# Optimization experiments

Hardware: AMD Instinct MI355X
Metric: run time of the kernel (lower is better)

The kernel has to match this reference:

```python
import jax, jax.numpy as jnp
import numpy as np

N = 50000
E = 800000
IN_CH = 128
HID = 16
HEADS = 8
OUT_CH = 64
NEG_SLOPE = 0.2


def _gat_conv(x, src, dst, W, a_src, a_dst, b, heads, ch):
    # x: [N, F_in]; W: [F_in, heads*ch]; a_src/a_dst: [heads, ch]; b: [heads*ch] or [ch]
    n = x.shape[0]
    h = (x @ W).reshape(n, heads, ch)                      # [N, H, C]
    s = jnp.einsum('nhc,hc->nh', h, a_src)                 # [N, H]
    d = jnp.einsum('nhc,hc->nh', h, a_dst)                 # [N, H]
    e = jax.nn.leaky_relu(s[src] + d[dst], NEG_SLOPE)      # [E, H]
    # numerically stable segment softmax over destination neighborhoods
    m = jax.ops.segment_max(e, dst, num_segments=n)        # [N, H]
    m = jnp.where(jnp.isfinite(m), m, 0.0)                 # guard isolated nodes
    w = jnp.exp(e - m[dst])                                # [E, H]
    z = jax.ops.segment_sum(w, dst, num_segments=n)        # [N, H]
    alpha = w / (z[dst] + 1e-16)                           # [E, H]
    msg = h[src] * alpha[:, :, None]                       # [E, H, C]
    out = jax.ops.segment_sum(msg, dst, num_segments=n)    # [N, H, C]
    return out.reshape(n, heads * ch) + b


def setup_inputs() -> dict:
    key = jax.random.key(0)
    ks = jax.random.split(key, 10)
    x = jax.random.normal(ks[0], (N, IN_CH), dtype=jnp.float32)
    edge_index = jax.random.randint(ks[1], (2, E), 0, N, dtype=jnp.int64)
    g1 = 1.0 / np.sqrt(IN_CH)
    g2 = 1.0 / np.sqrt(HEADS * HID)
    W1 = jax.random.normal(ks[2], (IN_CH, HEADS * HID), dtype=jnp.float32) * g1
    a_src1 = jax.random.normal(ks[3], (HEADS, HID), dtype=jnp.float32) * g2
    a_dst1 = jax.random.normal(ks[4], (HEADS, HID), dtype=jnp.float32) * g2
    b1 = jnp.zeros((HEADS * HID,), dtype=jnp.float32)
    W2 = jax.random.normal(ks[5], (HEADS * HID, OUT_CH), dtype=jnp.float32) * g2
    a_src2 = jax.random.normal(ks[6], (1, OUT_CH), dtype=jnp.float32) * (1.0 / np.sqrt(OUT_CH))
    a_dst2 = jax.random.normal(ks[7], (1, OUT_CH), dtype=jnp.float32) * (1.0 / np.sqrt(OUT_CH))
    b2 = jnp.zeros((OUT_CH,), dtype=jnp.float32)
    return {"x": x, "edge_index": edge_index,
            "W1": W1, "a_src1": a_src1, "a_dst1": a_dst1, "b1": b1,
            "W2": W2, "a_src2": a_src2, "a_dst2": a_dst2, "b2": b2}


def reference(x, edge_index, W1, a_src1, a_dst1, b1, W2, a_src2, a_dst2, b2):
    src, dst = edge_index[0], edge_index[1]
    # dropout layers are identity at inference
    h = _gat_conv(x, src, dst, W1, a_src1, a_dst1, b1, HEADS, HID)
    h = jax.nn.elu(h)
    out = _gat_conv(h, src, dst, W2, a_src2, a_dst2, b2, 1, OUT_CH)
    return out
```

## Files before the change

### kernel.cpp

```cpp
#include <hip/hip_runtime.h>
#include <hip/hip_fp16.h>

#define INCH   128
#define HEADS1 8
#define HID1   16
#define C1     128
#define C2     64
#define NEG_SLOPE 0.2f
#define SB     256

using f16x8 = __attribute__((ext_vector_type(8))) _Float16;
using f32x4 = __attribute__((ext_vector_type(4))) float;

__device__ __forceinline__ float lrelu(float v) { return v >= 0.f ? v : NEG_SLOPE * v; }
__device__ __forceinline__ int swzA(int row, int byteInRow) {
  return (row << 8) | (byteInRow ^ ((row & 15) << 4));
}


__global__ void prep_kernel(const float* __restrict__ x, __half* __restrict__ xh,
                            const float* __restrict__ W1, __half* __restrict__ W1t,
                            const float* __restrict__ W2, __half* __restrict__ W2t,
                            const int* __restrict__ dst, int* __restrict__ deg,
                            int cvtB, int tB, int total8, int E) {
  const int b = blockIdx.x, t = threadIdx.x;
  if (b < cvtB) {
    int i = b * 256 + t;
    if (i >= total8) return;
    const float4* p = (const float4*)x + (size_t)i * 2;
    float4 v0 = p[0], v1 = p[1];
    __half2 ha = __floats2half2_rn(v0.x, v0.y);
    __half2 hb = __floats2half2_rn(v0.z, v0.w);
    __half2 hc = __floats2half2_rn(v1.x, v1.y);
    __half2 hd = __floats2half2_rn(v1.z, v1.w);
    uint4 w = { *(unsigned*)&ha, *(unsigned*)&hb, *(unsigned*)&hc, *(unsigned*)&hd };
    ((uint4*)xh)[i] = w;
  } else if (b < cvtB + tB) {
    int id = (b - cvtB) * 256 + t;
    if (id < 128 * 128) {
      int col = id >> 7, k = id & 127;
      W1t[id] = __float2half(W1[k * 128 + col]);
    } else if (id < 128 * 128 + 64 * 128) {
      int idx = id - 128 * 128;
      int col = idx >> 7, k = idx & 127;
      W2t[idx] = __float2half(W2[k * 64 + col]);
    }
  } else {
    int e = (b - cvtB - tB) * 256 + t;
    if (e < E) atomicAdd(&deg[dst[e]], 1);
  }
}


__global__ void scan1_kernel(const int* __restrict__ deg, int* __restrict__ partial, int N) {
  __shared__ int sh[SB];
  const int b = blockIdx.x, t = threadIdx.x;
  const int chunk = (N + SB - 1) / SB;
  const int lo = b * chunk, hi = min(lo + chunk, N);
  int s = 0;
  for (int i = lo + t; i < hi; i += SB) s += deg[i];
  sh[t] = s;
  __syncthreads();
  for (int off = SB / 2; off; off >>= 1) {
    if (t < off) sh[t] += sh[t + off];
    __syncthreads();
  }
  if (t == 0) partial[b] = sh[0];
}

__global__ void scan3_kernel(const int* __restrict__ deg, const int* __restrict__ partial,
                             int* __restrict__ row_start, int N) {
  __shared__ int pref[SB];
  __shared__ int sh[SB];
  const int b = blockIdx.x, t = threadIdx.x;
  int pv = partial[t];
  pref[t] = pv;
  __syncthreads();
  for (int off = 1; off < SB; off <<= 1) {
    int u = (t >= off) ? pref[t - off] : 0;
    __syncthreads();
    pref[t] += u;
    __syncthreads();
  }
  const int chunk = (N + SB - 1) / SB;
  const int lo = b * chunk, hi = min(lo + chunk, N);
  int run = (b == 0) ? 0 : pref[b - 1];
  for (int base = lo; base < hi; base += SB) {
    int i = base + t;
    int v = (i < hi) ? deg[i] : 0;
    sh[t] = v;
    __syncthreads();
    for (int off = 1; off < SB; off <<= 1) {
      int u = (t >= off) ? sh[t - off] : 0;
      __syncthreads();
      sh[t] += u;
      __syncthreads();
    }
    if (i < hi) row_start[i] = run + sh[t] - v;
    run += sh[SB - 1];
    __syncthreads();
  }
  if (b == SB - 1 && t == 0) row_start[N] = run;
}

__global__ void fill_kernel(const int* __restrict__ src, const int* __restrict__ dst,
                            const int* __restrict__ row_start, int* __restrict__ cursor,
                            int* __restrict__ src_sorted, int E) {
  int e = blockIdx.x * blockDim.x + threadIdx.x;
  if (e >= E) return;
  int d = dst[e];
  int slot = row_start[d] + atomicAdd(&cursor[d], 1);
  src_sorted[slot] = src[e];
}

__global__ __launch_bounds__(256) void gemm1_mfma(
    const __half* __restrict__ xh, const __half* __restrict__ W1t,
    const float* __restrict__ a_src, const float* __restrict__ a_dst,
    __half* __restrict__ h1, float* __restrict__ s1, float* __restrict__ d1, int M) {
  __shared__ unsigned char As[16384];
  __shared__ unsigned char Bs[32768];
  const int t = threadIdx.x;
  const int m0 = blockIdx.x * 64;
  for (int c = t; c < 1024; c += 256) {
    int row = c >> 4, seg = c & 15;
    int gr = m0 + row;
    uint4 v = make_uint4(0, 0, 0, 0);
    if (gr < M) v = ((const uint4*)xh)[(unsigned)(gr << 4) + seg];
    *(uint4*)(As + swzA(row, seg << 4)) = v;
  }
  for (int c = t; c < 2048; c += 256) {
    int row = c >> 4, seg = c & 15;
    uint4 v = ((const uint4*)W1t)[(row << 4) + seg];
    *(uint4*)(Bs + swzA(row, seg << 4)) = v;
  }
  __syncthreads();
  const int l = t & 63, wid = t >> 6;
  const int c16 = l & 15;
  const int kOff = (l >> 4) << 4;
  const int rA = (wid << 4) | c16;
  f16x8 a[4];
#pragma unroll
  for (int kb = 0; kb < 4; ++kb)
    a[kb] = *(const f16x8*)(As + swzA(rA, (kb << 6) + kOff));
#pragma unroll
  for (int ct = 0; ct < 8; ++ct) {
    const int rB = (ct << 4) | c16;
    f32x4 acc = {0.f, 0.f, 0.f, 0.f};
#pragma unroll
    for (int kb = 0; kb < 4; ++kb) {
      f16x8 b = *(const f16x8*)(Bs + swzA(rB, (kb << 6) + kOff));
      acc = __builtin_amdgcn_mfma_f32_16x16x32_f16(a[kb], b, acc, 0, 0, 0);
    }
    const int colg = (ct << 4) + c16;
    const float asv = a_src[colg], adv = a_dst[colg];
#pragma unroll
    for (int i = 0; i < 4; ++i) {
      const int n = m0 + (wid << 4) + ((l >> 4) << 2) + i;
      float v = acc[i];
      float sv = v * asv, dv = v * adv;
      sv += __shfl_xor(sv, 1); sv += __shfl_xor(sv, 2);
      sv += __shfl_xor(sv, 4); sv += __shfl_xor(sv, 8);
      dv += __shfl_xor(dv, 1); dv += __shfl_xor(dv, 2);
      dv += __shfl_xor(dv, 4); dv += __shfl_xor(dv, 8);
      if (n < M) {
        h1[(unsigned)(n << 7) + colg] = __float2half(v);
        if (c16 == 0) { s1[n * HEADS1 + ct] = sv; d1[n * HEADS1 + ct] = dv; }
      }
    }
  }
}

__global__ __launch_bounds__(256) void gemm2_mfma(
    const __half* __restrict__ x2h, const __half* __restrict__ W2t,
    const float* __restrict__ a_src, const float* __restrict__ a_dst,
    __half* __restrict__ h2, float* __restrict__ s2, float* __restrict__ d2, int M) {
  __shared__ unsigned char As[16384];
  __shared__ unsigned char Bs[16384];
  const int t = threadIdx.x;
  const int m0 = blockIdx.x * 64;
  for (int c = t; c < 1024; c += 256) {
    int row = c >> 4, seg = c & 15;
    int gr = m0 + row;
    uint4 v = make_uint4(0, 0, 0, 0);
    if (gr < M) v = ((const uint4*)x2h)[(unsigned)(gr << 4) + seg];
    *(uint4*)(As + swzA(row, seg << 4)) = v;
  }
  for (int c = t; c < 1024; c += 256) {
    int row = c >> 4, seg = c & 15;
    uint4 v = ((const uint4*)W2t)[(row << 4) + seg];
    *(uint4*)(Bs + swzA(row, seg << 4)) = v;
  }
  __syncthreads();
  const int l = t & 63, wid = t >> 6;
  const int c16 = l & 15;
  const int kOff = (l >> 4) << 4;
  const int rA = (wid << 4) | c16;
  f16x8 a[4];
#pragma unroll
  for (int kb = 0; kb < 4; ++kb)
    a[kb] = *(const f16x8*)(As + swzA(rA, (kb << 6) + kOff));
  float svp[4] = {0.f, 0.f, 0.f, 0.f};
  float dvp[4] = {0.f, 0.f, 0.f, 0.f};
#pragma unroll
  for (int ct = 0; ct < 4; ++ct) {
    const int rB = (ct << 4) | c16;
    f32x4 acc = {0.f, 0.f, 0.f, 0.f};
#pragma unroll
    for (int kb = 0; kb < 4; ++kb) {
      f16x8 b = *(const f16x8*)(Bs + swzA(rB, (kb << 6) + kOff));
      acc = __builtin_amdgcn_mfma_f32_16x16x32_f16(a[kb], b, acc, 0, 0, 0);
    }
    const int colg = (ct << 4) + c16;
    const float asv = a_src[colg], adv = a_dst[colg];
#pragma unroll
    for (int i = 0; i < 4; ++i) {
      const int n = m0 + (wid << 4) + ((l >> 4) << 2) + i;
      float v = acc[i];
      svp[i] += v * asv;
      dvp[i] += v * adv;
      if (n < M) h2[(unsigned)(n << 6) + colg] = __float2half(v);
    }
  }
#pragma unroll
  for (int i = 0; i < 4; ++i) {
    float sv = svp[i], dv = dvp[i];
    sv += __shfl_xor(sv, 1); sv += __shfl_xor(sv, 2);
    sv += __shfl_xor(sv, 4); sv += __shfl_xor(sv, 8);
    dv += __shfl_xor(dv, 1); dv += __shfl_xor(dv, 2);
    dv += __shfl_xor(dv, 4); dv += __shfl_xor(dv, 8);
    const int n = m0 + (wid << 4) + ((l >> 4) << 2) + i;
    if (c16 == 0 && n < M) { s2[n] = sv; d2[n] = dv; }
  }
}

__global__ __launch_bounds__(256) void layer1_agg(
    const int* __restrict__ row_start, const int* __restrict__ src_sorted,
    const float* __restrict__ s1, const float* __restrict__ d1,
    const __half* __restrict__ h1, const float* __restrict__ b1,
    __half* __restrict__ x2h, int N) {
  __shared__ float wlds[4][64][8];
  const int wv = threadIdx.x >> 6;
  const int lane = threadIdx.x & 63;
  const int le = lane >> 3, h = lane & 7;
  const int es = lane >> 4, cl = lane & 15;
  const int hh = cl >> 1;
  const uint4* __restrict__ h1v = (const uint4*)h1;
  const int waveId = blockIdx.x * 4 + wv;
  const int stride = gridDim.x * 4;
  for (int n = waveId; n < N; n += stride) {
    const int lo = row_start[n], hi = row_start[n + 1];
    const float dv = d1[n * HEADS1 + h];
    float z = 0.f;
    float acc[8] = {0.f, 0.f, 0.f, 0.f, 0.f, 0.f, 0.f, 0.f};
    for (int base = lo; base < hi; base += 64) {
      const int cnt = min(64, hi - base);
      const int c1 = cnt - 1;
      const int j0 = le, j1 = 8 + le;
      const int sj0 = src_sorted[base + min(j0, c1)];
      const int sj1 = src_sorted[base + min(j1, c1)];
      const float sv0 = s1[sj0 * HEADS1 + h];
      const float sv1 = s1[sj1 * HEADS1 + h];
      const int ps0 = src_sorted[base + min(es, c1)];
      const int ps1 = src_sorted[base + min(4 + es, c1)];
      const int ps2 = src_sorted[base + min(8 + es, c1)];
      const int ps3 = src_sorted[base + min(12 + es, c1)];
      const uint4 pf0 = h1v[(unsigned)(ps0 << 4) + cl];
      const uint4 pf1 = h1v[(unsigned)(ps1 << 4) + cl];
      const uint4 pf2 = h1v[(unsigned)(ps2 << 4) + cl];
      const uint4 pf3 = h1v[(unsigned)(ps3 << 4) + cl];
      const float w0 = (j0 < cnt) ? __expf(lrelu(sv0 + dv)) : 0.f;
      const float w1 = (j1 < cnt) ? __expf(lrelu(sv1 + dv)) : 0.f;
      z += w0 + w1;
      const int rmax = (cnt + 7) >> 3;
      for (int r = 2; r < rmax; ++r) {
        const int j = (r << 3) + le;
        float w = 0.f;
        if (j < cnt) w = __expf(lrelu(s1[src_sorted[base + j] * HEADS1 + h] + dv));
        wlds[wv][j][h] = w;
        z += w;
      }
      {
        const float wA = __shfl(w0, (es << 3) | hh);
        const float wB = __shfl(w0, ((4 + es) << 3) | hh);
        const __half2* pA = (const __half2*)&pf0;
        const __half2* pB = (const __half2*)&pf1;
#pragma unroll
        for (int k = 0; k < 4; ++k) {
          float2 a2 = __half22float2(pA[k]);
          float2 b2v = __half22float2(pB[k]);
          acc[2 * k]     += wA * a2.x + wB * b2v.x;
          acc[2 * k + 1] += wA * a2.y + wB * b2v.y;
        }
      }
      if (cnt > 8) {
        const float wA = __shfl(w1, (es << 3) | hh);
        const float wB = __shfl(w1, ((4 + es) << 3) | hh);
        const __half2* pA = (const __half2*)&pf2;
        const __half2* pB = (const __half2*)&pf3;
#pragma unroll
        for (int k = 0; k < 4; ++k) {
          float2 a2 = __half22float2(pA[k]);
          float2 b2v = __half22float2(pB[k]);
          acc[2 * k]     += wA * a2.x + wB * b2v.x;
          acc[2 * k + 1] += wA * a2.y + wB * b2v.y;
        }
      }
      for (int i = 16; i < cnt; i += 8) {
        const int jA = i + es, jB = i + 4 + es;
        const float wA = wlds[wv][jA][hh];
        const float wB = wlds[wv][jB][hh];
        const int sA = src_sorted[base + min(jA, c1)];
        const int sB = src_sorted[base + min(jB, c1)];
        const uint4 fA = h1v[(unsigned)(sA << 4) + cl];
        const uint4 fB = h1v[(unsigned)(sB << 4) + cl];
        const __half2* pA = (const __half2*)&fA;
        const __half2* pB = (const __half2*)&fB;
#pragma unroll
        for (int k = 0; k < 4; ++k) {
          float2 a2 = __half22float2(pA[k]);
          float2 b2v = __half22float2(pB[k]);
          acc[2 * k]     += wA * a2.x + wB * b2v.x;
          acc[2 * k + 1] += wA * a2.y + wB * b2v.y;
        }
      }
    }
    z += __shfl_xor(z, 8); z += __shfl_xor(z, 16); z += __shfl_xor(z, 32);
    const float zsel = __shfl(z, hh);
#pragma unroll
    for (int k = 0; k < 8; ++k) {
      acc[k] += __shfl_xor(acc[k], 16);
      acc[k] += __shfl_xor(acc[k], 32);
    }
    if (es == 0) {
      const float zinv = 1.f / (zsel + 1e-16f);
      __half2 o[4];
#pragma unroll
      for (int k = 0; k < 4; ++k) {
        float ox = acc[2 * k] * zinv + b1[(cl << 3) + 2 * k];
        float oy = acc[2 * k + 1] * zinv + b1[(cl << 3) + 2 * k + 1];
        ox = ox > 0.f ? ox : expm1f(ox);
        oy = oy > 0.f ? oy : expm1f(oy);
        o[k] = __floats2half2_rn(ox, oy);
      }
      ((uint4*)x2h)[(unsigned)(n << 4) + cl] = *(const uint4*)o;
    }
  }
}

__global__ __launch_bounds__(256) void layer2_agg(
    const int* __restrict__ row_start, const int* __restrict__ src_sorted,
    const float* __restrict__ s2, const float* __restrict__ d2,
    const __half* __restrict__ h2, const float* __restrict__ b2,
    float* __restrict__ out, int N) {
  const int wv = threadIdx.x >> 6;
  const int lane = threadIdx.x & 63;
  const int es = lane >> 3, cl = lane & 7;
  const uint4* __restrict__ h2v = (const uint4*)h2;
  const int waveId = blockIdx.x * 4 + wv;
  const int stride = gridDim.x * 4;
  for (int n = waveId; n < N; n += stride) {
    const int lo = row_start[n], hi = row_start[n + 1];
    const float dv = d2[n];
    float z = 0.f;
    float acc[8] = {0.f, 0.f, 0.f, 0.f, 0.f, 0.f, 0.f, 0.f};
    for (int base = lo; base < hi; base += 64) {
      const int cnt = min(64, hi - base);
      const int c1 = cnt - 1;
      const int sidx = src_sorted[base + min(lane, c1)];
      const float sval = s2[sidx];
      const int ps0 = src_sorted[base + min(es, c1)];
      const int ps1 = src_sorted[base + min(8 + es, c1)];
      const int ps2 = src_sorted[base + min(16 + es, c1)];
      const int ps3 = src_sorted[base + min(24 + es, c1)];
      const uint4 pf0 = h2v[(unsigned)(ps0 << 3) + cl];
      const uint4 pf1 = h2v[(unsigned)(ps1 << 3) + cl];
      const uint4 pf2 = h2v[(unsigned)(ps2 << 3) + cl];
      const uint4 pf3 = h2v[(unsigned)(ps3 << 3) + cl];
      const float w = (lane < cnt) ? __expf(lrelu(sval + dv)) : 0.f;
      z += w;
      {
        const float wA = __shfl(w, es);
        const float wB = __shfl(w, 8 + es);
        const __half2* pA = (const __half2*)&pf0;
        const __half2* pB = (const __half2*)&pf1;
#pragma unroll
        for (int k = 0; k < 4; ++k) {
          float2 a2 = __half22float2(pA[k]);
          float2 b2v = __half22float2(pB[k]);
          acc[2 * k]     += wA * a2.x + wB * b2v.x;
          acc[2 * k + 1] += wA * a2.y + wB * b2v.y;
        }
      }
      if (cnt > 16) {
        const float wA = __shfl(w, 16 + es);
        const float wB = __shfl(w, 24 + es);
        const __half2* pA = (const __half2*)&pf2;
        const __half2* pB = (const __half2*)&pf3;
#pragma unroll
        for (int k = 0; k < 4; ++k) {
          float2 a2 = __half22float2(pA[k]);
          float2 b2v = __half22float2(pB[k]);
          acc[2 * k]     += wA * a2.x + wB * b2v.x;
          acc[2 * k + 1] += wA * a2.y + wB * b2v.y;
        }
      }
      for (int i = 32; i < cnt; i += 16) {
        const int jA = i + es, jB = i + 8 + es;
        const float wA = __shfl(w, jA);
        const float wB = __shfl(w, jB);
        const int sA = src_sorted[base + min(jA, c1)];
        const int sB = src_sorted[base + min(jB, c1)];
        const uint4 fA = h2v[(unsigned)(sA << 3) + cl];
        const uint4 fB = h2v[(unsigned)(sB << 3) + cl];
        const __half2* pA = (const __half2*)&fA;
        const __half2* pB = (const __half2*)&fB;
#pragma unroll
        for (int k = 0; k < 4; ++k) {
          float2 a2 = __half22float2(pA[k]);
          float2 b2v = __half22float2(pB[k]);
          acc[2 * k]     += wA * a2.x + wB * b2v.x;
          acc[2 * k + 1] += wA * a2.y + wB * b2v.y;
        }
      }
    }
#pragma unroll
    for (int off = 1; off < 64; off <<= 1) z += __shfl_xor(z, off);
#pragma unroll
    for (int k = 0; k < 8; ++k) {
      acc[k] += __shfl_xor(acc[k], 8);
      acc[k] += __shfl_xor(acc[k], 16);
      acc[k] += __shfl_xor(acc[k], 32);
    }
    if (es == 0) {
      const float zinv = 1.f / (z + 1e-16f);
      float4 o0, o1;
      o0.x = acc[0] * zinv + b2[(cl << 3) + 0];
      o0.y = acc[1] * zinv + b2[(cl << 3) + 1];
      o0.z = acc[2] * zinv + b2[(cl << 3) + 2];
      o0.w = acc[3] * zinv + b2[(cl << 3) + 3];
      o1.x = acc[4] * zinv + b2[(cl << 3) + 4];
      o1.y = acc[5] * zinv + b2[(cl << 3) + 5];
      o1.z = acc[6] * zinv + b2[(cl << 3) + 6];
      o1.w = acc[7] * zinv + b2[(cl << 3) + 7];
      float4* po = (float4*)&out[(unsigned)(n << 6) + (cl << 3)];
      po[0] = o0;
      po[1] = o1;
    }
  }
}

extern "C" void kernel_launch(void* const* d_in, const int* in_sizes, int n_in,
                              void* d_out, int out_size, void* d_ws, size_t ws_size,
                              hipStream_t stream) {
  const float* x      = (const float*)d_in[0];
  const int*   ei     = (const int*)d_in[1];
  const float* W1     = (const float*)d_in[2];
  const float* a_src1 = (const float*)d_in[3];
  const float* a_dst1 = (const float*)d_in[4];
  const float* b1     = (const float*)d_in[5];
  const float* W2     = (const float*)d_in[6];
  const float* a_src2 = (const float*)d_in[7];
  const float* a_dst2 = (const float*)d_in[8];
  const float* b2     = (const float*)d_in[9];
  float* out = (float*)d_out;

  const int N = in_sizes[0] / INCH;
  const int E = in_sizes[1] / 2;
  const int* src = ei;
  const int* dst = ei + E;

  float* ws = (float*)d_ws;
  size_t o = 0;
  __half* xh  = (__half*)(ws + o); o += (size_t)N * C1 / 2;
  __half* h1  = (__half*)(ws + o); o += (size_t)N * C1 / 2;
  __half* x2h = (__half*)(ws + o); o += (size_t)N * C1 / 2;
  float*  s1  = ws + o;            o += (size_t)N * HEADS1;
  float*  d1  = ws + o;            o += (size_t)N * HEADS1;
  __half* W1t = (__half*)(ws + o); o += 128 * 128 / 2;
  __half* W2t = (__half*)(ws + o); o += 64 * 128 / 2;
  int* deg        = (int*)(ws + o); o += N;
  int* cursor     = (int*)(ws + o); o += N;
  int* row_start  = (int*)(ws + o); o += N + 1;
  int* partial    = (int*)(ws + o); o += SB;
  int* src_sorted = (int*)(ws + o); o += E;
  __half* h2 = h1;
  float*  s2 = (float*)h1 + (size_t)N * 32;
  float*  d2 = s2 + N;

  const int EB = (E + 255) / 256;
  const int NB64 = (N + 63) / 64;
  const int total8 = N * C1 / 8;
  const int cvtB = (total8 + 255) / 256;
  const int tB = (128 * 128 + 64 * 128 + 255) / 256;
  const int histB = EB;
  const int AGGB = min((N + 3) / 4, 2048);

  hipMemsetAsync(deg, 0, (size_t)N * 4, stream);
  hipMemsetAsync(cursor, 0, (size_t)N * 4, stream);

  prep_kernel<<<cvtB + tB + histB, 256, 0, stream>>>(x, xh, W1, W1t, W2, W2t, dst, deg,
                                                     cvtB, tB, total8, E);
  scan1_kernel<<<SB, SB, 0, stream>>>(deg, partial, N);
  scan3_kernel<<<SB, SB, 0, stream>>>(deg, partial, row_start, N);
  fill_kernel<<<EB, 256, 0, stream>>>(src, dst, row_start, cursor, src_sorted, E);

  gemm1_mfma<<<NB64, 256, 0, stream>>>(xh, W1t, a_src1, a_dst1, h1, s1, d1, N);
  layer1_agg<<<AGGB, 256, 0, stream>>>(row_start, src_sorted, s1, d1, h1, b1, x2h, N);

  gemm2_mfma<<<NB64, 256, 0, stream>>>(x2h, W2t, a_src2, a_dst2, h2, s2, d2, N);
  layer2_agg<<<AGGB, 256, 0, stream>>>(row_start, src_sorted, s2, d2, h2, b2, out, N);
}
```

Before: 197.3 us.

## Fold attention vectors into extra GEMM columns and drop cursor memset

Precomputes W·a_src and W·a_dst as extra fp16 B-matrix columns so the attention logits s and d come straight out of one more MFMA tile, replacing the per-column multiply and shuffle reductions in both GEMM epilogues. The cursor array is now zeroed inside scan1 rather than by a separate memset. Logits are now computed from fp16-rounded folded weights, which changes numerics slightly, and each GEMM block issues one extra MFMA tile and loads a slightly larger shared B buffer.

```diff
diff --git a/kernel.cpp b/kernel.cpp
--- a/kernel.cpp
+++ b/kernel.cpp
@@ -17,10 +17,12 @@
   return (row << 8) | (byteInRow ^ ((row & 15) << 4));
 }
 
-
 __global__ void prep_kernel(const float* __restrict__ x, __half* __restrict__ xh,
                             const float* __restrict__ W1, __half* __restrict__ W1t,
                             const float* __restrict__ W2, __half* __restrict__ W2t,
+                            const float* __restrict__ a_src1, const float* __restrict__ a_dst1,
+                            const float* __restrict__ a_src2, const float* __restrict__ a_dst2,
+                            __half* __restrict__ B1e, __half* __restrict__ B2e,
                             const int* __restrict__ dst, int* __restrict__ deg,
                             int cvtB, int tB, int total8, int E) {
   const int b = blockIdx.x, t = threadIdx.x;
@@ -37,13 +39,34 @@
     ((uint4*)xh)[i] = w;
   } else if (b < cvtB + tB) {
     int id = (b - cvtB) * 256 + t;
-    if (id < 128 * 128) {
+    if (id < 16384) {
       int col = id >> 7, k = id & 127;
       W1t[id] = __float2half(W1[k * 128 + col]);
-    } else if (id < 128 * 128 + 64 * 128) {
-      int idx = id - 128 * 128;
+    } else if (id < 24576) {
+      int idx = id - 16384;
       int col = idx >> 7, k = idx & 127;
       W2t[idx] = __float2half(W2[k * 64 + col]);
+    } else if (id < 26624) {
+      int idx = id - 24576;
+      int col = idx >> 7, k = idx & 127;
+      const float* av = (col < 8) ? a_src1 : a_dst1;
+      int hh = col & 7;
+      float s = 0.f;
+#pragma unroll
+      for (int c = 0; c < 16; ++c) s += W1[k * 128 + hh * 16 + c] * av[hh * 16 + c];
+      B1e[col * 128 + k] = __float2half(s);
+    } else if (id < 28672) {
+      int idx = id - 26624;
+      int col = idx >> 7, k = idx & 127;
+      float s = 0.f;
+      if (col == 0) {
+#pragma unroll
+        for (int c = 0; c < 64; ++c) s += W2[k * 64 + c] * a_src2[c];
+      } else if (col == 1) {
+#pragma unroll
+        for (int c = 0; c < 64; ++c) s += W2[k * 64 + c] * a_dst2[c];
+      }
+      B2e[col * 128 + k] = __float2half(s);
     }
   } else {
     int e = (b - cvtB - tB) * 256 + t;
@@ -52,13 +75,17 @@
 }
 
 
-__global__ void scan1_kernel(const int* __restrict__ deg, int* __restrict__ partial, int N) {
+__global__ void scan1_kernel(const int* __restrict__ deg, int* __restrict__ partial,
+                             int* __restrict__ cursor, int N) {
   __shared__ int sh[SB];
   const int b = blockIdx.x, t = threadIdx.x;
   const int chunk = (N + SB - 1) / SB;
   const int lo = b * chunk, hi = min(lo + chunk, N);
   int s = 0;
-  for (int i = lo + t; i < hi; i += SB) s += deg[i];
+  for (int i = lo + t; i < hi; i += SB) {
+    s += deg[i];
+    cursor[i] = 0;
+  }
   sh[t] = s;
   __syncthreads();
   for (int off = SB / 2; off; off >>= 1) {
@@ -115,10 +142,10 @@
 
 __global__ __launch_bounds__(256) void gemm1_mfma(
     const __half* __restrict__ xh, const __half* __restrict__ W1t,
-    const float* __restrict__ a_src, const float* __restrict__ a_dst,
+    const __half* __restrict__ B1e,
     __half* __restrict__ h1, float* __restrict__ s1, float* __restrict__ d1, int M) {
   __shared__ unsigned char As[16384];
-  __shared__ unsigned char Bs[32768];
+  __shared__ unsigned char Bs[36864];
   const int t = threadIdx.x;
   const int m0 = blockIdx.x * 64;
   for (int c = t; c < 1024; c += 256) {
@@ -128,10 +155,15 @@
     if (gr < M) v = ((const uint4*)xh)[(unsigned)(gr << 4) + seg];
     *(uint4*)(As + swzA(row, seg << 4)) = v;
   }
-  for (int c = t; c < 2048; c += 256) {
+  for (int c = t; c < 2304; c += 256) {
     int row = c >> 4, seg = c & 15;
-    uint4 v = ((const uint4*)W1t)[(row << 4) + seg];
-    *(uint4*)(Bs + swzA(row, seg << 4)) = v;
+    if (row < 128) {
+      uint4 v = ((const uint4*)W1t)[(row << 4) + seg];
+      *(uint4*)(Bs + swzA(row, seg << 4)) = v;
+    } else {
+      uint4 v = ((const uint4*)B1e)[((row - 128) << 4) + seg];
+      *(uint4*)(Bs + 32768 + swzA(row - 128, seg << 4)) = v;
+    }
   }
   __syncthreads();
   const int l = t & 63, wid = t >> 6;
@@ -143,28 +175,30 @@
   for (int kb = 0; kb < 4; ++kb)
     a[kb] = *(const f16x8*)(As + swzA(rA, (kb << 6) + kOff));
 #pragma unroll
-  for (int ct = 0; ct < 8; ++ct) {
-    const int rB = (ct << 4) | c16;
+  for (int ct = 0; ct < 9; ++ct) {
+    const unsigned char* bbase = (ct < 8) ? Bs : (Bs + 32768);
+    const int rB = (ct < 8) ? ((ct << 4) | c16) : c16;
     f32x4 acc = {0.f, 0.f, 0.f, 0.f};
 #pragma unroll
     for (int kb = 0; kb < 4; ++kb) {
-      f16x8 b = *(const f16x8*)(Bs + swzA(rB, (kb << 6) + kOff));
+      f16x8 b = *(const f16x8*)(bbase + swzA(rB, (kb << 6) + kOff));
       acc = __builtin_amdgcn_mfma_f32_16x16x32_f16(a[kb], b, acc, 0, 0, 0);
     }
-    const int colg = (ct << 4) + c16;
-    const float asv = a_src[colg], adv = a_dst[colg];
-#pragma unroll
-    for (int i = 0; i < 4; ++i) {
-      const int n = m0 + (wid << 4) + ((l >> 4) << 2) + i;
-      float v = acc[i];
-      float sv = v * asv, dv = v * adv;
-      sv += __shfl_xor(sv, 1); sv += __shfl_xor(sv, 2);
-      sv += __shfl_xor(sv, 4); sv += __shfl_xor(sv, 8);
-      dv += __shfl_xor(dv, 1); dv += __shfl_xor(dv, 2);
-      dv += __shfl_xor(dv, 4); dv += __shfl_xor(dv, 8);
-      if (n < M) {
-        h1[(unsigned)(n << 7) + colg] = __float2half(v);
-        if (c16 == 0) { s1[n * HEADS1 + ct] = sv; d1[n * HEADS1 + ct] = dv; }
+    if (ct < 8) {
+      const int colg = (ct << 4) + c16;
+#pragma unroll
+      for (int i = 0; i < 4; ++i) {
+        const int n = m0 + (wid << 4) + ((l >> 4) << 2) + i;
+        if (n < M) h1[(unsigned)(n << 7) + colg] = __float2half(acc[i]);
+      }
+    } else {
+#pragma unroll
+      for (int i = 0; i < 4; ++i) {
+        const int n = m0 + (wid << 4) + ((l >> 4) << 2) + i;
+        if (n < M) {
+          if (c16 < 8) s1[n * HEADS1 + c16] = acc[i];
+          else         d1[n * HEADS1 + (c16 - 8)] = acc[i];
+        }
       }
     }
   }
@@ -172,10 +206,10 @@
 
 __global__ __launch_bounds__(256) void gemm2_mfma(
     const __half* __restrict__ x2h, const __half* __restrict__ W2t,
-    const float* __restrict__ a_src, const float* __restrict__ a_dst,
+    const __half* __restrict__ B2e,
     __half* __restrict__ h2, float* __restrict__ s2, float* __restrict__ d2, int M) {
   __shared__ unsigned char As[16384];
-  __shared__ unsigned char Bs[16384];
+  __shared__ unsigned char Bs[20480];
   const int t = threadIdx.x;
   const int m0 = blockIdx.x * 64;
   for (int c = t; c < 1024; c += 256) {
@@ -185,10 +219,15 @@
     if (gr < M) v = ((const uint4*)x2h)[(unsigned)(gr << 4) + seg];
     *(uint4*)(As + swzA(row, seg << 4)) = v;
   }
-  for (int c = t; c < 1024; c += 256) {
+  for (int c = t; c < 1280; c += 256) {
     int row = c >> 4, seg = c & 15;
-    uint4 v = ((const uint4*)W2t)[(row << 4) + seg];
-    *(uint4*)(Bs + swzA(row, seg << 4)) = v;
+    if (row < 64) {
+      uint4 v = ((const uint4*)W2t)[(row << 4) + seg];
+      *(uint4*)(Bs + swzA(row, seg << 4)) = v;
+    } else {
+      uint4 v = ((const uint4*)B2e)[((row - 64) << 4) + seg];
+      *(uint4*)(Bs + 16384 + swzA(row - 64, seg << 4)) = v;
+    }
   }
   __syncthreads();
   const int l = t & 63, wid = t >> 6;
@@ -199,37 +238,33 @@
 #pragma unroll
   for (int kb = 0; kb < 4; ++kb)
     a[kb] = *(const f16x8*)(As + swzA(rA, (kb << 6) + kOff));
-  float svp[4] = {0.f, 0.f, 0.f, 0.f};
-  float dvp[4] = {0.f, 0.f, 0.f, 0.f};
-#pragma unroll
-  for (int ct = 0; ct < 4; ++ct) {
-    const int rB = (ct << 4) | c16;
+#pragma unroll
+  for (int ct = 0; ct < 5; ++ct) {
+    const unsigned char* bbase = (ct < 4) ? Bs : (Bs + 16384);
+    const int rB = (ct < 4) ? ((ct << 4) | c16) : c16;
     f32x4 acc = {0.f, 0.f, 0.f, 0.f};
 #pragma unroll
     for (int kb = 0; kb < 4; ++kb) {
-      f16x8 b = *(const f16x8*)(Bs + swzA(rB, (kb << 6) + kOff));
+      f16x8 b = *(const f16x8*)(bbase + swzA(rB, (kb << 6) + kOff));
       acc = __builtin_amdgcn_mfma_f32_16x16x32_f16(a[kb], b, acc, 0, 0, 0);
     }
-    const int colg = (ct << 4) + c16;
-    const float asv = a_src[colg], adv = a_dst[colg];
-#pragma unroll
-    for (int i = 0; i < 4; ++i) {
-      const int n = m0 + (wid << 4) + ((l >> 4) << 2) + i;
-      float v = acc[i];
-      svp[i] += v * asv;
-      dvp[i] += v * adv;
-      if (n < M) h2[(unsigned)(n << 6) + colg] = __float2half(v);
-    }
-  }
-#pragma unroll
-  for (int i = 0; i < 4; ++i) {
-    float sv = svp[i], dv = dvp[i];
-    sv += __shfl_xor(sv, 1); sv += __shfl_xor(sv, 2);
-    sv += __shfl_xor(sv, 4); sv += __shfl_xor(sv, 8);
-    dv += __shfl_xor(dv, 1); dv += __shfl_xor(dv, 2);
-    dv += __shfl_xor(dv, 4); dv += __shfl_xor(dv, 8);
-    const int n = m0 + (wid << 4) + ((l >> 4) << 2) + i;
-    if (c16 == 0 && n < M) { s2[n] = sv; d2[n] = dv; }
+    if (ct < 4) {
+      const int colg = (ct << 4) + c16;
+#pragma unroll
+      for (int i = 0; i < 4; ++i) {
+        const int n = m0 + (wid << 4) + ((l >> 4) << 2) + i;
+        if (n < M) h2[(unsigned)(n << 6) + colg] = __float2half(acc[i]);
+      }
+    } else {
+#pragma unroll
+      for (int i = 0; i < 4; ++i) {
+        const int n = m0 + (wid << 4) + ((l >> 4) << 2) + i;
+        if (n < M) {
+          if (c16 == 0) s2[n] = acc[i];
+          else if (c16 == 1) d2[n] = acc[i];
+        }
+      }
+    }
   }
 }
 
@@ -478,6 +513,8 @@
   float*  d1  = ws + o;            o += (size_t)N * HEADS1;
   __half* W1t = (__half*)(ws + o); o += 128 * 128 / 2;
   __half* W2t = (__half*)(ws + o); o += 64 * 128 / 2;
+  __half* B1e = (__half*)(ws + o); o += 16 * 128 / 2;
+  __half* B2e = (__half*)(ws + o); o += 16 * 128 / 2;
   int* deg        = (int*)(ws + o); o += N;
   int* cursor     = (int*)(ws + o); o += N;
   int* row_start  = (int*)(ws + o); o += N + 1;
@@ -491,22 +528,22 @@
   const int NB64 = (N + 63) / 64;
   const int total8 = N * C1 / 8;
   const int cvtB = (total8 + 255) / 256;
-  const int tB = (128 * 128 + 64 * 128 + 255) / 256;
+  const int tB = (16384 + 8192 + 2048 + 2048) / 256;
   const int histB = EB;
   const int AGGB = min((N + 3) / 4, 2048);
 
   hipMemsetAsync(deg, 0, (size_t)N * 4, stream);
-  hipMemsetAsync(cursor, 0, (size_t)N * 4, stream);
-
-  prep_kernel<<<cvtB + tB + histB, 256, 0, stream>>>(x, xh, W1, W1t, W2, W2t, dst, deg,
-                                                     cvtB, tB, total8, E);
-  scan1_kernel<<<SB, SB, 0, stream>>>(deg, partial, N);
+
+  prep_kernel<<<cvtB + tB + histB, 256, 0, stream>>>(
+      x, xh, W1, W1t, W2, W2t, a_src1, a_dst1, a_src2, a_dst2, B1e, B2e,
+      dst, deg, cvtB, tB, total8, E);
+  scan1_kernel<<<SB, SB, 0, stream>>>(deg, partial, cursor, N);
   scan3_kernel<<<SB, SB, 0, stream>>>(deg, partial, row_start, N);
   fill_kernel<<<EB, 256, 0, stream>>>(src, dst, row_start, cursor, src_sorted, E);
 
-  gemm1_mfma<<<NB64, 256, 0, stream>>>(xh, W1t, a_src1, a_dst1, h1, s1, d1, N);
+  gemm1_mfma<<<NB64, 256, 0, stream>>>(xh, W1t, B1e, h1, s1, d1, N);
   layer1_agg<<<AGGB, 256, 0, stream>>>(row_start, src_sorted, s1, d1, h1, b1, x2h, N);
 
-  gemm2_mfma<<<NB64, 256, 0, stream>>>(x2h, W2t, a_src2, a_dst2, h2, s2, d2, N);
+  gemm2_mfma<<<NB64, 256, 0, stream>>>(x2h, W2t, B2e, h2, s2, d2, N);
   layer2_agg<<<AGGB, 256, 0, stream>>>(row_start, src_sorted, s2, d2, h2, b2, out, N);
 }
```

After: 186.4 us. 1.06x faster.
